# Kernel tuning notes

Hardware: AMD Instinct MI355X
Metric: run time of the kernel (lower is better)

Reference implementation:

```python
import jax, jax.numpy as jnp
import numpy as np

N = 50000       # num nodes
E = 800000      # num edges (before self loops)
D_IN = 128
D_H = 128
D_OUT = 40


def setup_inputs() -> dict:
    key = jax.random.key(0)
    ks = jax.random.split(key, 8)
    x = jax.random.normal(ks[0], (N, D_IN), dtype=jnp.float32)
    edge_index = jax.random.randint(ks[1], (2, E), 0, N, dtype=jnp.int32)
    # GCNConv weights (glorot-ish scale) and biases
    W1 = jax.random.normal(ks[2], (D_IN, D_H), dtype=jnp.float32) / np.sqrt(D_IN)
    b1 = jnp.zeros((D_H,), dtype=jnp.float32)
    W2 = jax.random.normal(ks[3], (D_H, D_H), dtype=jnp.float32) / np.sqrt(D_H)
    b2 = jnp.zeros((D_H,), dtype=jnp.float32)
    Wc = jax.random.normal(ks[4], (D_H, D_OUT), dtype=jnp.float32) / np.sqrt(D_H)
    bc = jnp.zeros((D_OUT,), dtype=jnp.float32)
    return {"x": x, "edge_index": edge_index, "W1": W1, "b1": b1,
            "W2": W2, "b2": b2, "Wc": Wc, "bc": bc}


def _gcn_conv(x, row, col, num_nodes, W, b):
    # PyG GCNConv: h = X @ W; out[c] += norm(r,c) * h[r]; out += b
    h = x @ W
    deg = jax.ops.segment_sum(jnp.ones(row.shape[0], h.dtype), col,
                              num_segments=num_nodes)
    dinv = jnp.where(deg > 0, jax.lax.rsqrt(deg), 0.0).astype(h.dtype)
    norm = dinv[row] * dinv[col]                      # [E+N]
    msg = h[row] * norm[:, None]                      # gather + scale
    agg = jax.ops.segment_sum(msg, col, num_segments=num_nodes)  # scatter-add
    return agg + b


def reference(x, edge_index, W1, b1, W2, b2, Wc, bc):
    # add self loops (GCNConv default add_self_loops=True)
    loops = jnp.arange(N, dtype=edge_index.dtype)
    row = jnp.concatenate([edge_index[0], loops])
    col = jnp.concatenate([edge_index[1], loops])
    h = jax.nn.relu(_gcn_conv(x, row, col, N, W1, b1))
    h = jax.nn.relu(_gcn_conv(h, row, col, N, W2, b2))
    g = jnp.mean(h, axis=0)                           # mean pool over nodes
    return g @ Wc + bc                                # [D_OUT]
```

## Files before the change

kernel.cpp:

```cpp
#include <hip/hip_runtime.h>
#include <hip/hip_fp16.h>


typedef _Float16 half8 __attribute__((ext_vector_type(8)));
typedef float f32x4 __attribute__((ext_vector_type(4)));
typedef float f32x2 __attribute__((ext_vector_type(2)));

constexpr int N = 50000;
constexpr int E = 800000;
constexpr int D = 128;
constexpr int DOUT = 40;
constexpr int CAP = 64;
constexpr int HB = 128;
constexpr int EPB = E / HB;
constexpr int HWRD = 12500;
constexpr int GM = (N + 127) / 128;
constexpr int NW = N / 4;
constexpr int T4 = E / 4;
constexpr int GF = 3 * GM;

__global__ __launch_bounds__(1024) void k_hist(const int* __restrict__ col,
                                               unsigned char* __restrict__ hist,
                                               unsigned char* __restrict__ rank,
                                               const float* __restrict__ W1,
                                               const float* __restrict__ W2,
                                               __half* __restrict__ T1,
                                               __half* __restrict__ T2) {
    __shared__ unsigned int h[HWRD];
    int b = blockIdx.x, t = threadIdx.x;
    if (b >= HB) {
        int o = (b - HB) * 1024 + t;
        const float* W = (o < 16384) ? W1 : W2;
        __half* T = (o < 16384) ? T1 : T2;
        int oo = o & 16383;
        int n = oo >> 7, k = oo & 127;
        T[oo] = (__half)W[k * 128 + n];
        return;
    }
    for (int i = t; i < HWRD; i += 1024) h[i] = 0;
    __syncthreads();
    int e0 = b * EPB;
    for (int e = e0 + t; e < e0 + EPB; e += 1024) {
        int c = col[e];
        unsigned int old = atomicAdd(&h[c >> 2], 1u << ((c & 3) * 8));
        rank[e] = (unsigned char)((old >> ((c & 3) * 8)) & 0xff);
    }
    __syncthreads();
    unsigned int* out = (unsigned int*)(hist + (size_t)b * 50000);
    for (int i = t; i < HWRD; i += 1024) out[i] = h[i];
}

__global__ void k_colscan(unsigned char* __restrict__ hist, int* __restrict__ deg,
                          float* __restrict__ dinv) {
    int c = blockIdx.x * 256 + threadIdx.x;
    if (c >= N) return;
    int sum = 0;
#pragma unroll 4
    for (int b = 0; b < HB; ++b) {
        size_t idx = (size_t)b * 50000 + c;
        int v = hist[idx];
        hist[idx] = (unsigned char)sum;
        sum += v;
    }
    deg[c] = sum;
    dinv[c] = rsqrtf((float)(sum + 1));
}

__device__ __forceinline__ unsigned char f8enc(float v) {
    return (unsigned char)(__builtin_amdgcn_cvt_pk_fp8_f32(v, v, 0, false) & 0xff);
}
__device__ __forceinline__ void add8f8(float* a, uint2 u) {
    f32x2 f0 = __builtin_amdgcn_cvt_pk_f32_fp8(u.x, false);
    f32x2 f1 = __builtin_amdgcn_cvt_pk_f32_fp8(u.x, true);
    f32x2 f2 = __builtin_amdgcn_cvt_pk_f32_fp8(u.y, false);
    f32x2 f3 = __builtin_amdgcn_cvt_pk_f32_fp8(u.y, true);
    a[0] += f0[0]; a[1] += f0[1]; a[2] += f1[0]; a[3] += f1[1];
    a[4] += f2[0]; a[5] += f2[1]; a[6] += f3[0]; a[7] += f3[1];
}

__device__ __forceinline__ half8 ldA(const float* rowp, int koff) {
    float4 u0 = *(const float4*)(rowp + koff);
    float4 u1 = *(const float4*)(rowp + koff + 4);
    half8 r;
    r[0] = (_Float16)u0.x; r[1] = (_Float16)u0.y;
    r[2] = (_Float16)u0.z; r[3] = (_Float16)u0.w;
    r[4] = (_Float16)u1.x; r[5] = (_Float16)u1.y;
    r[6] = (_Float16)u1.z; r[7] = (_Float16)u1.w;
    return r;
}
__device__ __forceinline__ half8 ldA(const __half* rowp, int koff) {
    return *(const half8*)(rowp + koff);
}

template <typename TA>
__device__ __forceinline__ void mfma_gemm(const TA* __restrict__ A,
                                          const __half* __restrict__ Wt,
                                          const float* __restrict__ dinv,
                                          unsigned char* __restrict__ out8,
                                          int row0, int tid) {
    int wave = tid >> 6, lane = tid & 63;
    int quad = lane >> 4, c16 = lane & 15;
    int m0 = row0 + wave * 32;
    int ra = m0 + c16;      if (ra >= N) ra = 0;
    int rb = m0 + 16 + c16; if (rb >= N) rb = 0;
    const TA* pa = A + (size_t)ra * D;
    const TA* pb = A + (size_t)rb * D;

    f32x4 acc[2][8];
#pragma unroll
    for (int i = 0; i < 2; ++i)
#pragma unroll
        for (int j = 0; j < 8; ++j) acc[i][j] = (f32x4){0.f, 0.f, 0.f, 0.f};

#pragma unroll
    for (int kq = 0; kq < 4; ++kq) {
        int koff = kq * 32 + quad * 8;
        half8 a0 = ldA(pa, koff);
        half8 a1 = ldA(pb, koff);
#pragma unroll
        for (int nt = 0; nt < 8; ++nt) {
            half8 bf = *(const half8*)(Wt + (size_t)(nt * 16 + c16) * D + koff);
            acc[0][nt] = __builtin_amdgcn_mfma_f32_16x16x32_f16(a0, bf, acc[0][nt], 0, 0, 0);
            acc[1][nt] = __builtin_amdgcn_mfma_f32_16x16x32_f16(a1, bf, acc[1][nt], 0, 0, 0);
        }
    }

#pragma unroll
    for (int rt = 0; rt < 2; ++rt) {
        int mt = m0 + rt * 16;
#pragma unroll
        for (int i = 0; i < 4; ++i) {
            int grow = mt + quad * 4 + i;
            if (grow < N) {
                float s = dinv[grow];
                unsigned char* orow = out8 + (size_t)grow * D + c16;
#pragma unroll
                for (int nt = 0; nt < 8; ++nt)
                    orow[nt * 16] = f8enc(acc[rt][nt][i] * s);
            }
        }
    }
}

__global__ __launch_bounds__(256) void k_fuse(const int* __restrict__ ei,
                                              const unsigned char* __restrict__ hist,
                                              const unsigned char* __restrict__ rank,
                                              unsigned short* __restrict__ csr,
                                              const float* __restrict__ x,
                                              const __half* __restrict__ Wt1,
                                              const float* __restrict__ dinv,
                                              unsigned char* __restrict__ out8) {
    int b = blockIdx.x, m = b % 3;
    if (m < 2) {
        int sb = (b / 3) * 2 + m;
        int t = sb * 256 + threadIdx.x;
        if (t >= T4) return;
#pragma unroll
        for (int i = 0; i < 4; ++i) {
            int e = t + i * T4;
            int c = ei[E + e];
            int r = ei[e];
            int chunk = e / EPB;
            int slot = (int)hist[(size_t)chunk * 50000 + c] + (int)rank[e];
            if (slot < CAP) csr[(c << 6) + slot] = (unsigned short)r;
        }
        return;
    }
    mfma_gemm<float>(x, Wt1, dinv, out8, (b / 3) * 128, threadIdx.x);
}

__global__ __launch_bounds__(256) void k_gemm(const __half* __restrict__ A,
                                              const __half* __restrict__ Wt,
                                              const float* __restrict__ dinv,
                                              unsigned char* __restrict__ out8) {
    mfma_gemm<__half>(A, Wt, dinv, out8, blockIdx.x * 128, threadIdx.x);
}

__device__ __forceinline__ float agg_core(int c, int lane,
                                          const unsigned char* __restrict__ hs8,
                                          const int* __restrict__ deg,
                                          const unsigned short* __restrict__ csr,
                                          float* a0) {
    int qw = lane >> 4;
    int q  = lane & 15;
    int dgRaw = deg[c];
    int dg = dgRaw < CAP ? dgRaw : CAP;
    float dc = rsqrtf((float)(dgRaw + 1));
    int e0 = c << 6;

    float a1[8] = {0, 0, 0, 0, 0, 0, 0, 0};
    float a2[8] = {0, 0, 0, 0, 0, 0, 0, 0};
    float a3[8] = {0, 0, 0, 0, 0, 0, 0, 0};
#pragma unroll
    for (int t = 0; t < 8; ++t) a0[t] = 0.f;
    if (qw == 0)
        add8f8(a0, *(const uint2*)&hs8[(size_t)c * D + q * 8]);

    int j = 0;
    for (; j + 16 <= dg; j += 16) {
        int r0 = csr[e0 + j + qw];
        int r1 = csr[e0 + j + 4 + qw];
        int r2 = csr[e0 + j + 8 + qw];
        int r3 = csr[e0 + j + 12 + qw];
        uint2 u0 = *(const uint2*)&hs8[(size_t)r0 * D + q * 8];
        uint2 u1 = *(const uint2*)&hs8[(size_t)r1 * D + q * 8];
        uint2 u2 = *(const uint2*)&hs8[(size_t)r2 * D + q * 8];
        uint2 u3 = *(const uint2*)&hs8[(size_t)r3 * D + q * 8];
        add8f8(a0, u0); add8f8(a1, u1); add8f8(a2, u2); add8f8(a3, u3);
    }
    if (j + 8 <= dg) {
        int r0 = csr[e0 + j + qw];
        int r1 = csr[e0 + j + 4 + qw];
        uint2 u0 = *(const uint2*)&hs8[(size_t)r0 * D + q * 8];
        uint2 u1 = *(const uint2*)&hs8[(size_t)r1 * D + q * 8];
        add8f8(a0, u0); add8f8(a1, u1);
        j += 8;
    }
    if (j + 4 <= dg) {
        int r0 = csr[e0 + j + qw];
        add8f8(a0, *(const uint2*)&hs8[(size_t)r0 * D + q * 8]);
        j += 4;
    }
    int rem = dg - j;
    if (qw < rem) {
        int r0 = csr[e0 + j + qw];
        add8f8(a1, *(const uint2*)&hs8[(size_t)r0 * D + q * 8]);
    }

#pragma unroll
    for (int t = 0; t < 8; ++t) a0[t] += a1[t];
#pragma unroll
    for (int t = 0; t < 8; ++t) a2[t] += a3[t];
#pragma unroll
    for (int t = 0; t < 8; ++t) a0[t] += a2[t];
#pragma unroll
    for (int t = 0; t < 8; ++t) a0[t] += __shfl_xor(a0[t], 16, 64);
#pragma unroll
    for (int t = 0; t < 8; ++t) a0[t] += __shfl_xor(a0[t], 32, 64);
    return dc;
}

__global__ __launch_bounds__(256) void k_agg1(const unsigned char* __restrict__ hs8,
                                              const int* __restrict__ deg,
                                              const unsigned short* __restrict__ csr,
                                              const float* __restrict__ bias,
                                              __half* __restrict__ outH) {
    int wave = threadIdx.x >> 6;
    int lane = threadIdx.x & 63;
    int c = blockIdx.x * 4 + wave;
    float a0[8];
    float dc = agg_core(c, lane, hs8, deg, csr, a0);
    if ((lane >> 4) == 0) {
        int q = lane & 15;
        union { __half2 h[4]; uint4 u; } p;
#pragma unroll
        for (int i = 0; i < 4; ++i) {
            float xv = fmaxf(fmaf(dc, a0[2 * i],     bias[q * 8 + 2 * i]),     0.f);
            float yv = fmaxf(fmaf(dc, a0[2 * i + 1], bias[q * 8 + 2 * i + 1]), 0.f);
            p.h[i] = __floats2half2_rn(xv, yv);
        }
        *(uint4*)&outH[(size_t)c * D + q * 8] = p.u;
    }
}

__global__ __launch_bounds__(256) void k_agg2(const unsigned char* __restrict__ hs8,
                                              const int* __restrict__ deg,
                                              const unsigned short* __restrict__ csr,
                                              const float* __restrict__ bias,
                                              float* __restrict__ gpart) {
    __shared__ float gblk[4][128];
    int wave = threadIdx.x >> 6;
    int lane = threadIdx.x & 63;
    int c = blockIdx.x * 4 + wave;
    float a0[8];
    float dc = agg_core(c, lane, hs8, deg, csr, a0);
    if ((lane >> 4) == 0) {
        int q = lane & 15;
#pragma unroll
        for (int i = 0; i < 8; ++i)
            gblk[wave][q * 8 + i] = fmaxf(fmaf(dc, a0[i], bias[q * 8 + i]), 0.f);
    }
    __syncthreads();
    int t = threadIdx.x;
    if (t < 128)
        gpart[(size_t)blockIdx.x * 128 + t] =
            gblk[0][t] + gblk[1][t] + gblk[2][t] + gblk[3][t];
}

__global__ __launch_bounds__(256) void k_pool(const float* __restrict__ gpart,
                                              float* __restrict__ gpart2) {
    int d = threadIdx.x & 127;
    int half = threadIdx.x >> 7;
    int b = blockIdx.x;
    int per = (NW + 255) / 256;
    int r0 = b * per;
    int r1 = r0 + per;
    if (r1 > NW) r1 = NW;
    float acc = 0.f;
    for (int r = r0 + half; r < r1; r += 2)
        acc += gpart[(size_t)r * D + d];
    __shared__ float red[256];
    red[threadIdx.x] = acc;
    __syncthreads();
    if (half == 0) gpart2[(size_t)b * D + d] = red[d] + red[128 + d];
}

__global__ __launch_bounds__(512) void k_final(const float* __restrict__ gpart2,
                                               const float* __restrict__ Wc,
                                               const float* __restrict__ bc,
                                               float* __restrict__ out) {
    __shared__ float g[D];
    __shared__ float red[512];
    int t = threadIdx.x;
    int d = t & 127, grp = t >> 7;
    float s = 0.f;
#pragma unroll 4
    for (int w = grp * 64; w < grp * 64 + 64; ++w)
        s += gpart2[(size_t)w * D + d];
    red[t] = s;
    __syncthreads();
    if (grp == 0)
        g[d] = (red[d] + red[128 + d] + red[256 + d] + red[384 + d]) * (1.0f / (float)N);
    __syncthreads();
    if (t < DOUT) {
        float acc = bc[t];
        for (int dd = 0; dd < D; ++dd) acc = fmaf(g[dd], Wc[dd * DOUT + t], acc);
        out[t] = acc;
    }
}

extern "C" void kernel_launch(void* const* d_in, const int* in_sizes, int n_in,
                              void* d_out, int out_size, void* d_ws, size_t ws_size,
                              hipStream_t stream) {
    const float* x  = (const float*)d_in[0];
    const int*   ei = (const int*)d_in[1];
    const float* W1 = (const float*)d_in[2];
    const float* b1 = (const float*)d_in[3];
    const float* W2 = (const float*)d_in[4];
    const float* b2 = (const float*)d_in[5];
    const float* Wc = (const float*)d_in[6];
    const float* bc = (const float*)d_in[7];
    float* out = (float*)d_out;

    char* ws = (char*)d_ws;
    size_t off = 0;
    auto alloc = [&](size_t bytes) {
        void* p = ws + off;
        off += (bytes + 511) & ~(size_t)511;
        return p;
    };
    unsigned char*  hist   = (unsigned char*) alloc((size_t)HB * 50000);
    unsigned char*  rank   = (unsigned char*) alloc((size_t)E);
    int*            deg    = (int*)           alloc((size_t)N * 4);
    float*          dinv   = (float*)         alloc((size_t)N * 4);
    unsigned short* csr    = (unsigned short*)alloc((size_t)N * CAP * 2);
    unsigned char*  hs8    = (unsigned char*) alloc((size_t)N * D);
    __half*         hactH  = (__half*)        alloc((size_t)N * D * 2);
    __half*         Wt1    = (__half*)        alloc((size_t)D * D * 2);
    __half*         Wt2    = (__half*)        alloc((size_t)D * D * 2);
    float*          gpart  = (float*)         alloc((size_t)NW * D * 4);
    float*          gpart2 = (float*)         alloc((size_t)256 * D * 4);
    (void)ws_size; (void)in_sizes; (void)n_in; (void)out_size;

    const int* col = ei + E;

    k_hist<<<HB + 32, 1024, 0, stream>>>(col, hist, rank, W1, W2, Wt1, Wt2);
    k_colscan<<<(N + 255) / 256, 256, 0, stream>>>(hist, deg, dinv);
    k_fuse<<<GF, 256, 0, stream>>>(ei, hist, rank, csr, x, Wt1, dinv, hs8);

    k_agg1<<<NW, 256, 0, stream>>>(hs8, deg, csr, b1, hactH);
    k_gemm<<<GM, 256, 0, stream>>>(hactH, Wt2, dinv, hs8);
    k_agg2<<<NW, 256, 0, stream>>>(hs8, deg, csr, b2, gpart);
    k_pool<<<256, 256, 0, stream>>>(gpart, gpart2);
    k_final<<<1, 512, 0, stream>>>(gpart2, Wc, bc, out);
}
```

Before: 213.3 us.

## Split fp8 feature table into two 64-column planes for aggregation locality

New measurement: 235.3 us. 1.1x slower.

```diff
diff --git a/kernel.cpp b/kernel.cpp
--- a/kernel.cpp
+++ b/kernel.cpp
@@ -15,9 +15,11 @@
 constexpr int EPB = E / HB;
 constexpr int HWRD = 12500;
 constexpr int GM = (N + 127) / 128;
-constexpr int NW = N / 4;
+constexpr int NQ = N / 4;
+constexpr int GA = NQ * 2;
 constexpr int T4 = E / 4;
 constexpr int GF = 3 * GM;
+constexpr int PSTRIDE = N * 64;
 
 __global__ __launch_bounds__(1024) void k_hist(const int* __restrict__ col,
                                                unsigned char* __restrict__ hist,
@@ -133,10 +135,13 @@
             int grow = mt + quad * 4 + i;
             if (grow < N) {
                 float s = dinv[grow];
-                unsigned char* orow = out8 + (size_t)grow * D + c16;
-#pragma unroll
-                for (int nt = 0; nt < 8; ++nt)
-                    orow[nt * 16] = f8enc(acc[rt][nt][i] * s);
+                unsigned char* o0 = out8 + (size_t)grow * 64 + c16;
+                unsigned char* o1 = o0 + PSTRIDE;
+#pragma unroll
+                for (int nt = 0; nt < 4; ++nt) {
+                    o0[nt * 16] = f8enc(acc[rt][nt][i] * s);
+                    o1[nt * 16] = f8enc(acc[rt][nt + 4][i] * s);
+                }
             }
         }
     }
@@ -177,67 +182,56 @@
 }
 
 __device__ __forceinline__ float agg_core(int c, int lane,
-                                          const unsigned char* __restrict__ hs8,
+                                          const unsigned char* __restrict__ hs8p,
                                           const int* __restrict__ deg,
                                           const unsigned short* __restrict__ csr,
                                           float* a0) {
-    int qw = lane >> 4;
-    int q  = lane & 15;
+    int g  = lane >> 3;
+    int q8 = lane & 7;
     int dgRaw = deg[c];
     int dg = dgRaw < CAP ? dgRaw : CAP;
     float dc = rsqrtf((float)(dgRaw + 1));
     int e0 = c << 6;
 
     float a1[8] = {0, 0, 0, 0, 0, 0, 0, 0};
-    float a2[8] = {0, 0, 0, 0, 0, 0, 0, 0};
-    float a3[8] = {0, 0, 0, 0, 0, 0, 0, 0};
 #pragma unroll
     for (int t = 0; t < 8; ++t) a0[t] = 0.f;
-    if (qw == 0)
-        add8f8(a0, *(const uint2*)&hs8[(size_t)c * D + q * 8]);
+    if (g == 0)
+        add8f8(a0, *(const uint2*)&hs8p[(size_t)c * 64 + q8 * 8]);
 
     int j = 0;
     for (; j + 16 <= dg; j += 16) {
-        int r0 = csr[e0 + j + qw];
-        int r1 = csr[e0 + j + 4 + qw];
-        int r2 = csr[e0 + j + 8 + qw];
-        int r3 = csr[e0 + j + 12 + qw];
-        uint2 u0 = *(const uint2*)&hs8[(size_t)r0 * D + q * 8];
-        uint2 u1 = *(const uint2*)&hs8[(size_t)r1 * D + q * 8];
-        uint2 u2 = *(const uint2*)&hs8[(size_t)r2 * D + q * 8];
-        uint2 u3 = *(const uint2*)&hs8[(size_t)r3 * D + q * 8];
-        add8f8(a0, u0); add8f8(a1, u1); add8f8(a2, u2); add8f8(a3, u3);
+        int r0 = csr[e0 + j + g];
+        int r1 = csr[e0 + j + 8 + g];
+        uint2 u0 = *(const uint2*)&hs8p[(size_t)r0 * 64 + q8 * 8];
+        uint2 u1 = *(const uint2*)&hs8p[(size_t)r1 * 64 + q8 * 8];
+        add8f8(a0, u0); add8f8(a1, u1);
     }
     if (j + 8 <= dg) {
-        int r0 = csr[e0 + j + qw];
-        int r1 = csr[e0 + j + 4 + qw];
-        uint2 u0 = *(const uint2*)&hs8[(size_t)r0 * D + q * 8];
-        uint2 u1 = *(const uint2*)&hs8[(size_t)r1 * D + q * 8];
-        add8f8(a0, u0); add8f8(a1, u1);
+        int r0 = csr[e0 + j + g];
+        add8f8(a0, *(const uint2*)&hs8p[(size_t)r0 * 64 + q8 * 8]);
         j += 8;
     }
-    if (j + 4 <= dg) {
-        int r0 = csr[e0 + j + qw];
-        add8f8(a0, *(const uint2*)&hs8[(size_t)r0 * D + q * 8]);
-        j += 4;
-    }
     int rem = dg - j;
-    if (qw < rem) {
-        int r0 = csr[e0 + j + qw];
-        add8f8(a1, *(const uint2*)&hs8[(size_t)r0 * D + q * 8]);
+    if (g < rem) {
+        int r0 = csr[e0 + j + g];
+        add8f8(a1, *(const uint2*)&hs8p[(size_t)r0 * 64 + q8 * 8]);
     }
 
 #pragma unroll
     for (int t = 0; t < 8; ++t) a0[t] += a1[t];
 #pragma unroll
-    for (int t = 0; t < 8; ++t) a2[t] += a3[t];
-#pragma unroll
-    for (int t = 0; t < 8; ++t) a0[t] += a2[t];
+    for (int t = 0; t < 8; ++t) a0[t] += __shfl_xor(a0[t], 8, 64);
 #pragma unroll
     for (int t = 0; t < 8; ++t) a0[t] += __shfl_xor(a0[t], 16, 64);
 #pragma unroll
     for (int t = 0; t < 8; ++t) a0[t] += __shfl_xor(a0[t], 32, 64);
     return dc;
+}
+
+__device__ __forceinline__ void agg_idx(int b, int& quad, int& p) {
+    p = ((b & 7) >> 2);
+    quad = (b >> 3) * 4 + (b & 3);
 }
 
 __global__ __launch_bounds__(256) void k_agg1(const unsigned char* __restrict__ hs8,
@@ -245,21 +239,25 @@
                                               const unsigned short* __restrict__ csr,
                                               const float* __restrict__ bias,
                                               __half* __restrict__ outH) {
+    int quad, p;
+    agg_idx(blockIdx.x, quad, p);
     int wave = threadIdx.x >> 6;
     int lane = threadIdx.x & 63;
-    int c = blockIdx.x * 4 + wave;
+    int c = quad * 4 + wave;
+    const unsigned char* hs8p = hs8 + (size_t)p * PSTRIDE;
     float a0[8];
-    float dc = agg_core(c, lane, hs8, deg, csr, a0);
-    if ((lane >> 4) == 0) {
-        int q = lane & 15;
-        union { __half2 h[4]; uint4 u; } p;
+    float dc = agg_core(c, lane, hs8p, deg, csr, a0);
+    if ((lane >> 3) == 0) {
+        int q8 = lane & 7;
+        int cb = p * 64 + q8 * 8;
+        union { __half2 h[4]; uint4 u; } pk;
 #pragma unroll
         for (int i = 0; i < 4; ++i) {
-            float xv = fmaxf(fmaf(dc, a0[2 * i],     bias[q * 8 + 2 * i]),     0.f);
-            float yv = fmaxf(fmaf(dc, a0[2 * i + 1], bias[q * 8 + 2 * i + 1]), 0.f);
-            p.h[i] = __floats2half2_rn(xv, yv);
+            float xv = fmaxf(fmaf(dc, a0[2 * i],     bias[cb + 2 * i]),     0.f);
+            float yv = fmaxf(fmaf(dc, a0[2 * i + 1], bias[cb + 2 * i + 1]), 0.f);
+            pk.h[i] = __floats2half2_rn(xv, yv);
         }
-        *(uint4*)&outH[(size_t)c * D + q * 8] = p.u;
+        *(uint4*)&outH[(size_t)c * D + cb] = pk.u;
     }
 }
 
@@ -268,22 +266,26 @@
                                               const unsigned short* __restrict__ csr,
                                               const float* __restrict__ bias,
                                               float* __restrict__ gpart) {
-    __shared__ float gblk[4][128];
+    __shared__ float gblk[4][64];
+    int quad, p;
+    agg_idx(blockIdx.x, quad, p);
     int wave = threadIdx.x >> 6;
     int lane = threadIdx.x & 63;
-    int c = blockIdx.x * 4 + wave;
+    int c = quad * 4 + wave;
+    const unsigned char* hs8p = hs8 + (size_t)p * PSTRIDE;
     float a0[8];
-    float dc = agg_core(c, lane, hs8, deg, csr, a0);
-    if ((lane >> 4) == 0) {
-        int q = lane & 15;
+    float dc = agg_core(c, lane, hs8p, deg, csr, a0);
+    if ((lane >> 3) == 0) {
+        int q8 = lane & 7;
+        int cb = p * 64 + q8 * 8;
 #pragma unroll
         for (int i = 0; i < 8; ++i)
-            gblk[wave][q * 8 + i] = fmaxf(fmaf(dc, a0[i], bias[q * 8 + i]), 0.f);
+            gblk[wave][q8 * 8 + i] = fmaxf(fmaf(dc, a0[i], bias[cb + i]), 0.f);
     }
     __syncthreads();
     int t = threadIdx.x;
-    if (t < 128)
-        gpart[(size_t)blockIdx.x * 128 + t] =
+    if (t < 64)
+        gpart[(size_t)quad * 128 + p * 64 + t] =
             gblk[0][t] + gblk[1][t] + gblk[2][t] + gblk[3][t];
 }
 
@@ -292,10 +294,10 @@
     int d = threadIdx.x & 127;
     int half = threadIdx.x >> 7;
     int b = blockIdx.x;
-    int per = (NW + 255) / 256;
+    int per = (NQ + 255) / 256;
     int r0 = b * per;
     int r1 = r0 + per;
-    if (r1 > NW) r1 = NW;
+    if (r1 > NQ) r1 = NQ;
     float acc = 0.f;
     for (int r = r0 + half; r < r1; r += 2)
         acc += gpart[(size_t)r * D + d];
@@ -358,7 +360,7 @@
     __half*         hactH  = (__half*)        alloc((size_t)N * D * 2);
     __half*         Wt1    = (__half*)        alloc((size_t)D * D * 2);
     __half*         Wt2    = (__half*)        alloc((size_t)D * D * 2);
-    float*          gpart  = (float*)         alloc((size_t)NW * D * 4);
+    float*          gpart  = (float*)         alloc((size_t)NQ * D * 4);
     float*          gpart2 = (float*)         alloc((size_t)256 * D * 4);
     (void)ws_size; (void)in_sizes; (void)n_in; (void)out_size;
 
@@ -368,9 +370,9 @@
     k_colscan<<<(N + 255) / 256, 256, 0, stream>>>(hist, deg, dinv);
     k_fuse<<<GF, 256, 0, stream>>>(ei, hist, rank, csr, x, Wt1, dinv, hs8);
 
-    k_agg1<<<NW, 256, 0, stream>>>(hs8, deg, csr, b1, hactH);
+    k_agg1<<<GA, 256, 0, stream>>>(hs8, deg, csr, b1, hactH);
     k_gemm<<<GM, 256, 0, stream>>>(hactH, Wt2, dinv, hs8);
-    k_agg2<<<NW, 256, 0, stream>>>(hs8, deg, csr, b2, gpart);
+    k_agg2<<<GA, 256, 0, stream>>>(hs8, deg, csr, b2, gpart);
     k_pool<<<256, 256, 0, stream>>>(gpart, gpart2);
     k_final<<<1, 512, 0, stream>>>(gpart2, Wc, bc, out);
 }
```
